# Kernel optimization log

Hardware: AMD Instinct MI355X
Metric: run time of the kernel (lower is better)

## Reference

```python
import jax, jax.numpy as jnp
import numpy as np

LN_EPS = 1e-5
NEG_INF = -1e38


def wkv_scan(w, u, k, v):
    """Numerically-stable RWKV WKV recurrence (matches wkv_cuda forward).
    w: [C] (negative decay), u: [C] bonus, k/v: [B,T,C]. Returns y: [B,T,C]."""
    Bdim, T, C = k.shape

    def step(carry, kv_t):
        p, q, o = carry  # running num, den, log-scale, each [B,C]
        kt, vt = kv_t
        no = jnp.maximum(o, u + kt)
        A = jnp.exp(o - no)
        Bw = jnp.exp(u + kt - no)
        y = (A * p + Bw * vt) / (A * q + Bw)
        no2 = jnp.maximum(w + o, kt)
        A2 = jnp.exp(w + o - no2)
        B2 = jnp.exp(kt - no2)
        return (A2 * p + B2 * vt, A2 * q + B2, no2), y

    init = (jnp.zeros((Bdim, C), k.dtype), jnp.zeros((Bdim, C), k.dtype),
            jnp.full((Bdim, C), NEG_INF, k.dtype))
    kT = jnp.moveaxis(k, 1, 0)  # [T,B,C]
    vT = jnp.moveaxis(v, 1, 0)
    _, ys = jax.lax.scan(step, init, (kT, vT))
    return jnp.moveaxis(ys, 0, 1)  # [B,T,C]


def setup_inputs() -> dict:
    key = jax.random.key(0)
    ks = jax.random.split(key, 8)
    B, C, H, W = 16, 192, 56, 56
    s = 0.02
    x = jax.random.normal(ks[0], (B, C, H, W), jnp.float32)
    Wk = jax.random.normal(ks[1], (C, C), jnp.float32) * s
    Wv = jax.random.normal(ks[2], (C, C), jnp.float32) * s
    Wr = jax.random.normal(ks[3], (C, C), jnp.float32) * s
    Wo = jax.random.normal(ks[4], (C, C), jnp.float32) * s
    ln_g = jnp.ones((C,), jnp.float32)
    ln_b = jnp.zeros((C,), jnp.float32)
    w_decay = -6.0 + 0.1 * jax.random.normal(ks[5], (C,), jnp.float32)
    u = 0.1 * jax.random.normal(ks[6], (C,), jnp.float32)
    return {"x": x, "Wk": Wk, "Wv": Wv, "Wr": Wr, "Wo": Wo,
            "ln_g": ln_g, "ln_b": ln_b, "w_decay": w_decay, "u": u}


def reference(x, Wk, Wv, Wr, Wo, ln_g, ln_b, w_decay, u):
    B, C, H, W = x.shape
    xs = jnp.transpose(x.reshape(B, C, H * W), (0, 2, 1))  # [B,T,C]
    k = jnp.einsum('btc,dc->btd', xs, Wk)
    v = jnp.einsum('btc,dc->btd', xs, Wv)
    r = jnp.einsum('btc,dc->btd', xs, Wr)
    real_w = -jnp.exp(w_decay)
    x_fwd = wkv_scan(real_w, u, k, v)
    x_bwd = jnp.flip(wkv_scan(real_w, u, jnp.flip(k, 1), jnp.flip(v, 1)), 1)
    x_bi = 0.5 * (x_fwd + x_bwd)
    h = jax.nn.sigmoid(r) * x_bi
    mu = jnp.mean(h, axis=-1, keepdims=True)
    var = jnp.var(h, axis=-1, keepdims=True)
    h = (h - mu) * jax.lax.rsqrt(var + LN_EPS) * ln_g + ln_b
    out = jnp.einsum('btc,dc->btd', h, Wo)  # dropout is identity at eval
    return jnp.transpose(out, (0, 2, 1)).reshape(B, C, H, W)
```

## Files before the change

kernel.cpp:

```cpp
#include <hip/hip_runtime.h>
#include <hip/hip_bf16.h>

#define BB 16
#define CC 192
#define TPIX 3136
#define NCH 49
#define CHL 64
#define NNELE ((size_t)BB * TPIX * CC)
#define NSTATE ((size_t)2 * BB * NCH * CC)
#define WCH (CC * CC)

typedef __attribute__((ext_vector_type(8))) short bf16x8;
typedef __attribute__((ext_vector_type(4))) float f32x4;
typedef __attribute__((ext_vector_type(16))) float f32x16;

__device__ __forceinline__ unsigned short f2bf(float f) {
    __hip_bfloat16 b = __float2bfloat16(f);
    return *reinterpret_cast<unsigned short*>(&b);
}
__device__ __forceinline__ float bf2f(unsigned short h) {
    union { unsigned u; float f; } v; v.u = ((unsigned)h) << 16;
    return v.f;
}


__global__ __launch_bounds__(256) void wcvt_frag(
    const float* __restrict__ Wk, const float* __restrict__ Wv,
    const float* __restrict__ Wr, const float* __restrict__ Wo,
    unsigned short* __restrict__ wfrag)
{
    const int id = blockIdx.x * 256 + threadIdx.x;
    const int m = id / 4608;
    const int r = id % 4608;
    const int tile = r >> 6;
    const int lane = r & 63;
    const int dr = tile / 12, tk = tile % 12;
    const int d = dr * 32 + (lane & 31);
    const int c = tk * 16 + (lane >> 5) * 8;
    const float* W = (m == 0) ? Wk : (m == 1) ? Wv : (m == 2) ? Wr : Wo;
    const float4 a = *(const float4*)&W[d * CC + c];
    const float4 b = *(const float4*)&W[d * CC + c + 4];
    bf16x8 o;
    o[0] = (short)f2bf(a.x); o[1] = (short)f2bf(a.y);
    o[2] = (short)f2bf(a.z); o[3] = (short)f2bf(a.w);
    o[4] = (short)f2bf(b.x); o[5] = (short)f2bf(b.y);
    o[6] = (short)f2bf(b.z); o[7] = (short)f2bf(b.w);
    *(bf16x8*)&wfrag[(size_t)m * WCH + (size_t)tile * 512 + lane * 8] = o;
}

__global__ __launch_bounds__(256) void xcvt_frag(
    const float* __restrict__ x, unsigned short* __restrict__ xfrag)
{
    const int t0 = blockIdx.x * 32;
    const int b  = blockIdx.y;
    __shared__ float ls[CC][33];
    const int tid = threadIdx.x;
#pragma unroll
    for (int it = 0; it < 6; ++it) {
        const int c  = it * 32 + (tid >> 3);
        const int t4 = (tid & 7) * 4;
        *(float4*)&ls[c][t4] =
            *(const float4*)&x[((size_t)b * CC + c) * TPIX + t0 + t4];
    }
    __syncthreads();
    const size_t tbase = ((size_t)(b * TPIX + t0) >> 5) * 12;
#pragma unroll
    for (int it = 0; it < 3; ++it) {
        const int id = it * 256 + tid;
        const int tk = id >> 6;
        const int lane = id & 63;
        const int r32 = lane & 31;
        const int c0 = tk * 16 + (lane >> 5) * 8;
        bf16x8 o;
#pragma unroll
        for (int e = 0; e < 8; ++e)
            o[e] = (short)f2bf(ls[c0 + e][r32]);
        *(bf16x8*)&xfrag[(tbase + tk) * 512 + lane * 8] = o;
    }
}

__global__ __launch_bounds__(512, 4) void proj_mfma32(
    const unsigned short* __restrict__ xfrag,
    const unsigned short* __restrict__ wfrag,
    unsigned short* __restrict__ kbf, unsigned short* __restrict__ vbf,
    unsigned short* __restrict__ rbf)
{
    __shared__ unsigned short wlds[WCH];
    const int tid  = threadIdx.x;
    const int lane = tid & 63;
    const int wv   = tid >> 6;
    const int tw   = wv >> 1;
    const int dwav = wv & 1;
    const int l31  = lane & 31;
    const int kh   = lane >> 5;
    const int m    = blockIdx.z;

    const size_t row0 = (size_t)blockIdx.x * 128 + tw * 32;
    const size_t xtb  = (row0 >> 5) * 12;

    bf16x8 xf[12];
#pragma unroll
    for (int ks = 0; ks < 12; ++ks)
        xf[ks] = *(const bf16x8*)&xfrag[(xtb + ks) * 512 + lane * 8];

    const unsigned short* wm = wfrag + (size_t)m * WCH;
#pragma unroll
    for (int it = 0; it < 9; ++it) {
        const int off = (it * 512 + tid) * 8;
        *(bf16x8*)&wlds[off] = *(const bf16x8*)&wm[off];
    }
    __syncthreads();

    f32x16 acc[3];
#pragma unroll
    for (int nn = 0; nn < 3; ++nn)
#pragma unroll
        for (int e = 0; e < 16; ++e) acc[nn][e] = 0.f;

#pragma unroll
    for (int ks = 0; ks < 12; ++ks) {
        bf16x8 wf[3];
#pragma unroll
        for (int nn = 0; nn < 3; ++nn)
            wf[nn] = *(const bf16x8*)&wlds[((dwav * 3 + nn) * 12 + ks) * 512 + lane * 8];
#pragma unroll
        for (int nn = 0; nn < 3; ++nn)
            acc[nn] = __builtin_amdgcn_mfma_f32_32x32x16_bf16(
                xf[ks], wf[nn], acc[nn], 0, 0, 0);
    }

    unsigned short* om = (m == 0) ? kbf : (m == 1) ? vbf : rbf;
#pragma unroll
    for (int nn = 0; nn < 3; ++nn) {
        const int d = dwav * 96 + nn * 32 + l31;
#pragma unroll
        for (int q = 0; q < 16; ++q) {
            const int t = (q & 3) + 8 * (q >> 2) + 4 * kh;
            om[(row0 + t) * CC + d] = f2bf(acc[nn][q]);
        }
    }
}

__global__ __launch_bounds__(512, 4) void outproj_mfma32(
    const unsigned short* __restrict__ hfrag,
    const unsigned short* __restrict__ wo,
    float* __restrict__ out)
{
    __shared__ unsigned short wlds[WCH];
    const int tid  = threadIdx.x;
    const int lane = tid & 63;
    const int wv   = tid >> 6;
    const int tw   = wv >> 1;
    const int dwav = wv & 1;
    const int l31  = lane & 31;
    const int kh   = lane >> 5;

    const size_t row0 = (size_t)blockIdx.x * 128 + tw * 32;
    const size_t htb  = (row0 >> 5) * 12;

    bf16x8 hf[12];
#pragma unroll
    for (int ks = 0; ks < 12; ++ks)
        hf[ks] = *(const bf16x8*)&hfrag[(htb + ks) * 512 + lane * 8];

#pragma unroll
    for (int it = 0; it < 9; ++it) {
        const int off = (it * 512 + tid) * 8;
        *(bf16x8*)&wlds[off] = *(const bf16x8*)&wo[off];
    }
    __syncthreads();

    f32x16 acc[3];
#pragma unroll
    for (int nn = 0; nn < 3; ++nn)
#pragma unroll
        for (int e = 0; e < 16; ++e) acc[nn][e] = 0.f;

#pragma unroll
    for (int ks = 0; ks < 12; ++ks) {
        bf16x8 wf[3];
#pragma unroll
        for (int nn = 0; nn < 3; ++nn)
            wf[nn] = *(const bf16x8*)&wlds[((dwav * 3 + nn) * 12 + ks) * 512 + lane * 8];
#pragma unroll
        for (int nn = 0; nn < 3; ++nn)
            acc[nn] = __builtin_amdgcn_mfma_f32_32x32x16_bf16(
                hf[ks], wf[nn], acc[nn], 0, 0, 0);
    }

#pragma unroll
    for (int nn = 0; nn < 3; ++nn) {
        const int d = dwav * 96 + nn * 32 + l31;
#pragma unroll
        for (int q2 = 0; q2 < 4; ++q2) {
            const size_t grow = row0 + 4 * kh + 8 * q2;
            const int b  = (int)(grow / TPIX);
            const int tl = (int)(grow % TPIX);
            f32x4 v4 = {acc[nn][q2 * 4 + 0], acc[nn][q2 * 4 + 1],
                        acc[nn][q2 * 4 + 2], acc[nn][q2 * 4 + 3]};
            *(f32x4*)&out[((size_t)b * CC + d) * TPIX + tl] = v4;
        }
    }
}

__global__ __launch_bounds__(256) void wkv_chunk_kernel(
    const unsigned short* __restrict__ kb, const unsigned short* __restrict__ vb,
    const float* __restrict__ wdec,
    float* __restrict__ sp, float* __restrict__ sq, float* __restrict__ so)
{
    const int gid = blockIdx.x * 256 + threadIdx.x;
    const int c  = gid % CC;
    const int r  = gid / CC;
    const int ch = r % NCH;
    const int r2 = r / NCH;
    const int b  = r2 % BB;
    const int dir = r2 / BB;

    const float w = -__expf(wdec[c]);
    const int tstart = dir ? (TPIX - 1 - ch * CHL) : (ch * CHL);
    const long stride = dir ? -(long)CC : (long)CC;
    long idx = ((long)b * TPIX + tstart) * CC + c;

    float p = 0.f, q = 0.f, o = -1e38f;
#pragma unroll 4
    for (int j = 0; j < CHL; ++j) {
        const float kt = bf2f(kb[idx]), vt = bf2f(vb[idx]);
        const float wo  = w + o;
        const float no2 = fmaxf(wo, kt);
        const float A2  = __expf(wo - no2);
        const float B2  = __expf(kt - no2);
        p = A2 * p + B2 * vt;
        q = A2 * q + B2;
        o = no2;
        idx += stride;
    }
    sp[gid] = p; sq[gid] = q; so[gid] = o;
}

__global__ __launch_bounds__(256) void wkv_prefix_kernel(
    float* __restrict__ sp, float* __restrict__ sq, float* __restrict__ so,
    const float* __restrict__ wdec)
{
    const int tid = blockIdx.x * 256 + threadIdx.x;
    if (tid >= 2 * BB * CC) return;
    const int c = tid % CC;
    const int g = tid / CC;
    const float w  = -__expf(wdec[c]);
    const float wL = w * CHL;

    float P = 0.f, Q = 0.f, O = -1e38f;
    size_t idx = (size_t)g * NCH * CC + c;
    for (int ch = 0; ch < NCH; ++ch) {
        const float pl = sp[idx], ql = sq[idx], ol = so[idx];
        sp[idx] = P; sq[idx] = Q; so[idx] = O;
        const float Ow = O + wL;
        const float no = fmaxf(Ow, ol);
        const float A  = __expf(Ow - no);
        const float Bf = __expf(ol - no);
        P = A * P + Bf * pl;
        Q = A * Q + Bf * ql;
        O = no;
        idx += CC;
    }
}

__global__ __launch_bounds__(256) void wkv_emit_kernel(
    const unsigned short* __restrict__ kb, const unsigned short* __restrict__ vb,
    const float* __restrict__ wdec, const float* __restrict__ ubias,
    const float* __restrict__ sp, const float* __restrict__ sq,
    const float* __restrict__ so,
    unsigned short* __restrict__ yfwd, unsigned short* __restrict__ ybwd)
{
    const int gid = blockIdx.x * 256 + threadIdx.x;
    const int c  = gid % CC;
    const int r  = gid / CC;
    const int ch = r % NCH;
    const int r2 = r / NCH;
    const int b  = r2 % BB;
    const int dir = r2 / BB;

    const float w = -__expf(wdec[c]);
    const float u = ubias[c];
    const int tstart = dir ? (TPIX - 1 - ch * CHL) : (ch * CHL);
    const long stride = dir ? -(long)CC : (long)CC;
    long idx = ((long)b * TPIX + tstart) * CC + c;
    unsigned short* yout = dir ? ybwd : yfwd;

    float p = sp[gid], q = sq[gid], o = so[gid];
#pragma unroll 2
    for (int j = 0; j < CHL; ++j) {
        const float kt = bf2f(kb[idx]), vt = bf2f(vb[idx]);
        const float uk  = u + kt;
        const float no  = fmaxf(o, uk);
        const float A   = __expf(o - no);
        const float Bw  = __expf(uk - no);
        const float num = A * p + Bw * vt;
        const float den = A * q + Bw;
        yout[idx] = f2bf(0.5f * __fdividef(num, den));
        const float wo  = w + o;
        const float no2 = fmaxf(wo, kt);
        const float A2  = __expf(wo - no2);
        const float B2  = __expf(kt - no2);
        p = A2 * p + B2 * vt;
        q = A2 * q + B2;
        o = no2;
        idx += stride;
    }
}

__global__ __launch_bounds__(192) void ln_kernel(
    const unsigned short* __restrict__ rbf,
    const unsigned short* __restrict__ yfwd, const unsigned short* __restrict__ ybwd,
    const float* __restrict__ gamma, const float* __restrict__ beta,
    unsigned short* __restrict__ hfrag)
{
    const size_t row = blockIdx.x;
    const int c = threadIdx.x;
    const size_t idx = row * CC + c;
    const float rv = bf2f(rbf[idx]);
    const float xb = bf2f(yfwd[idx]) + bf2f(ybwd[idx]);
    const float hv = xb / (1.f + __expf(-rv));
    float s = hv, s2 = hv * hv;
#pragma unroll
    for (int off = 1; off < 64; off <<= 1) {
        s  += __shfl_xor(s, off);
        s2 += __shfl_xor(s2, off);
    }
    __shared__ float red[2][3];
    const int wv = threadIdx.x >> 6;
    if ((threadIdx.x & 63) == 0) { red[0][wv] = s; red[1][wv] = s2; }
    __syncthreads();
    s  = red[0][0] + red[0][1] + red[0][2];
    s2 = red[1][0] + red[1][1] + red[1][2];
    const float mu   = s * (1.f / CC);
    const float var  = s2 * (1.f / CC) - mu * mu;
    const float rstd = rsqrtf(var + 1e-5f);
    const float hval = (hv - mu) * rstd * gamma[c] + beta[c];
    const size_t off = ((row >> 5) * 12 + (c >> 4)) * 512 +
                       ((row & 31) + ((c >> 3) & 1) * 32) * 8 + (c & 7);
    hfrag[off] = f2bf(hval);
}

extern "C" void kernel_launch(void* const* d_in, const int* in_sizes, int n_in,
                              void* d_out, int out_size, void* d_ws, size_t ws_size,
                              hipStream_t stream)
{
    const float* x    = (const float*)d_in[0];
    const float* Wk   = (const float*)d_in[1];
    const float* Wv   = (const float*)d_in[2];
    const float* Wr   = (const float*)d_in[3];
    const float* Wo   = (const float*)d_in[4];
    const float* ln_g = (const float*)d_in[5];
    const float* ln_b = (const float*)d_in[6];
    const float* wdec = (const float*)d_in[7];
    const float* u    = (const float*)d_in[8];

    unsigned short* kbf   = (unsigned short*)d_ws;
    unsigned short* vbf   = kbf + NNELE;
    unsigned short* rbf   = vbf + NNELE;
    unsigned short* xfrag = rbf + NNELE;
    unsigned short* wfrag = xfrag + NNELE;
    float* sp = (float*)xfrag;
    float* sq = sp + NSTATE;
    float* so = sq + NSTATE;
    unsigned short* hfrag = kbf;
    unsigned short* yfwd  = (unsigned short*)d_out;
    unsigned short* ybwd  = yfwd + NNELE;
    float* out = (float*)d_out;

    wcvt_frag<<<72, 256, 0, stream>>>(Wk, Wv, Wr, Wo, wfrag);
    xcvt_frag<<<dim3(TPIX / 32, BB), 256, 0, stream>>>(x, xfrag);

    proj_mfma32<<<dim3((BB * TPIX) / 128, 1, 3), 512, 0, stream>>>(
        xfrag, wfrag, kbf, vbf, rbf);

    const int nth = (int)NSTATE;
    wkv_chunk_kernel<<<nth / 256, 256, 0, stream>>>(kbf, vbf, wdec, sp, sq, so);
    wkv_prefix_kernel<<<(2 * BB * CC + 255) / 256, 256, 0, stream>>>(sp, sq, so, wdec);
    wkv_emit_kernel<<<nth / 256, 256, 0, stream>>>(kbf, vbf, wdec, u, sp, sq, so, yfwd, ybwd);

    ln_kernel<<<BB * TPIX, 192, 0, stream>>>(rbf, yfwd, ybwd, ln_g, ln_b, hfrag);

    outproj_mfma32<<<(BB * TPIX) / 128, 512, 0, stream>>>(hfrag, wfrag + 3 * WCH, out);
}
```

Baseline: 135.6 us.

## Fuse sigmoid-gate LayerNorm into output projection using MFMA fragment layout

The separate LayerNorm kernel is removed and its work moved into the output-projection MFMA kernel. To make this possible, the r projection and the WKV emit outputs are now written directly in the MFMA A-fragment layout. Each lane computes the gated value h for its 96 channels, and one shuffle across the two half-waves gives the row statistics. This drops a full-size launch and the hfrag round trip through memory. In exchange the emit kernel and the r projection now do scattered 2-byte stores, yfwd and ybwd move from the output buffer to the workspace, and h is rounded to bf16 before normalisation.

```diff
diff --git a/kernel.cpp b/kernel.cpp
--- a/kernel.cpp
+++ b/kernel.cpp
@@ -83,7 +83,7 @@
     const unsigned short* __restrict__ xfrag,
     const unsigned short* __restrict__ wfrag,
     unsigned short* __restrict__ kbf, unsigned short* __restrict__ vbf,
-    unsigned short* __restrict__ rbf)
+    unsigned short* __restrict__ rfrag)
 {
     __shared__ unsigned short wlds[WCH];
     const int tid  = threadIdx.x;
@@ -129,76 +129,28 @@
                 xf[ks], wf[nn], acc[nn], 0, 0, 0);
     }
 
-    unsigned short* om = (m == 0) ? kbf : (m == 1) ? vbf : rbf;
-#pragma unroll
-    for (int nn = 0; nn < 3; ++nn) {
-        const int d = dwav * 96 + nn * 32 + l31;
-#pragma unroll
-        for (int q = 0; q < 16; ++q) {
-            const int t = (q & 3) + 8 * (q >> 2) + 4 * kh;
-            om[(row0 + t) * CC + d] = f2bf(acc[nn][q]);
+    if (m == 2) {
+#pragma unroll
+        for (int nn = 0; nn < 3; ++nn) {
+            const int d = dwav * 96 + nn * 32 + l31;
+            const size_t tb = ((row0 >> 5) * 12 + (d >> 4)) * 512 +
+                              (size_t)(((d >> 3) & 1) * 32) * 8 + (d & 7);
+#pragma unroll
+            for (int q = 0; q < 16; ++q) {
+                const int tq = (q & 3) + 8 * (q >> 2) + 4 * kh;
+                rfrag[tb + tq * 8] = f2bf(acc[nn][q]);
+            }
         }
-    }
-}
-
-__global__ __launch_bounds__(512, 4) void outproj_mfma32(
-    const unsigned short* __restrict__ hfrag,
-    const unsigned short* __restrict__ wo,
-    float* __restrict__ out)
-{
-    __shared__ unsigned short wlds[WCH];
-    const int tid  = threadIdx.x;
-    const int lane = tid & 63;
-    const int wv   = tid >> 6;
-    const int tw   = wv >> 1;
-    const int dwav = wv & 1;
-    const int l31  = lane & 31;
-    const int kh   = lane >> 5;
-
-    const size_t row0 = (size_t)blockIdx.x * 128 + tw * 32;
-    const size_t htb  = (row0 >> 5) * 12;
-
-    bf16x8 hf[12];
-#pragma unroll
-    for (int ks = 0; ks < 12; ++ks)
-        hf[ks] = *(const bf16x8*)&hfrag[(htb + ks) * 512 + lane * 8];
-
-#pragma unroll
-    for (int it = 0; it < 9; ++it) {
-        const int off = (it * 512 + tid) * 8;
-        *(bf16x8*)&wlds[off] = *(const bf16x8*)&wo[off];
-    }
-    __syncthreads();
-
-    f32x16 acc[3];
-#pragma unroll
-    for (int nn = 0; nn < 3; ++nn)
-#pragma unroll
-        for (int e = 0; e < 16; ++e) acc[nn][e] = 0.f;
-
-#pragma unroll
-    for (int ks = 0; ks < 12; ++ks) {
-        bf16x8 wf[3];
-#pragma unroll
-        for (int nn = 0; nn < 3; ++nn)
-            wf[nn] = *(const bf16x8*)&wlds[((dwav * 3 + nn) * 12 + ks) * 512 + lane * 8];
-#pragma unroll
-        for (int nn = 0; nn < 3; ++nn)
-            acc[nn] = __builtin_amdgcn_mfma_f32_32x32x16_bf16(
-                hf[ks], wf[nn], acc[nn], 0, 0, 0);
-    }
-
-#pragma unroll
-    for (int nn = 0; nn < 3; ++nn) {
-        const int d = dwav * 96 + nn * 32 + l31;
-#pragma unroll
-        for (int q2 = 0; q2 < 4; ++q2) {
-            const size_t grow = row0 + 4 * kh + 8 * q2;
-            const int b  = (int)(grow / TPIX);
-            const int tl = (int)(grow % TPIX);
-            f32x4 v4 = {acc[nn][q2 * 4 + 0], acc[nn][q2 * 4 + 1],
-                        acc[nn][q2 * 4 + 2], acc[nn][q2 * 4 + 3]};
-            *(f32x4*)&out[((size_t)b * CC + d) * TPIX + tl] = v4;
+    } else {
+        unsigned short* om = (m == 0) ? kbf : vbf;
+#pragma unroll
+        for (int nn = 0; nn < 3; ++nn) {
+            const int d = dwav * 96 + nn * 32 + l31;
+#pragma unroll
+            for (int q = 0; q < 16; ++q) {
+                const int t = (q & 3) + 8 * (q >> 2) + 4 * kh;
+                om[(row0 + t) * CC + d] = f2bf(acc[nn][q]);
+            }
         }
     }
 }
@@ -283,8 +235,13 @@
     const float u = ubias[c];
     const int tstart = dir ? (TPIX - 1 - ch * CHL) : (ch * CHL);
     const long stride = dir ? -(long)CC : (long)CC;
+    const int rstep = dir ? -1 : 1;
     long idx = ((long)b * TPIX + tstart) * CC + c;
+    long row = (long)b * TPIX + tstart;
     unsigned short* yout = dir ? ybwd : yfwd;
+    const int ctile = c >> 4;
+    const int clane = ((c >> 3) & 1) * 32;
+    const int ce    = c & 7;
 
     float p = sp[gid], q = sq[gid], o = so[gid];
 #pragma unroll 2
@@ -296,7 +253,9 @@
         const float Bw  = __expf(uk - no);
         const float num = A * p + Bw * vt;
         const float den = A * q + Bw;
-        yout[idx] = f2bf(0.5f * __fdividef(num, den));
+        const size_t off = ((size_t)(row >> 5) * 12 + ctile) * 512 +
+                           (size_t)((row & 31) + clane) * 8 + ce;
+        yout[off] = f2bf(0.5f * __fdividef(num, den));
         const float wo  = w + o;
         const float no2 = fmaxf(wo, kt);
         const float A2  = __expf(wo - no2);
@@ -305,40 +264,113 @@
         q = A2 * q + B2;
         o = no2;
         idx += stride;
-    }
-}
-
-__global__ __launch_bounds__(192) void ln_kernel(
-    const unsigned short* __restrict__ rbf,
+        row += rstep;
+    }
+}
+
+__global__ __launch_bounds__(512) void outproj_ln_mfma32(
     const unsigned short* __restrict__ yfwd, const unsigned short* __restrict__ ybwd,
+    const unsigned short* __restrict__ rfrag,
     const float* __restrict__ gamma, const float* __restrict__ beta,
-    unsigned short* __restrict__ hfrag)
-{
-    const size_t row = blockIdx.x;
-    const int c = threadIdx.x;
-    const size_t idx = row * CC + c;
-    const float rv = bf2f(rbf[idx]);
-    const float xb = bf2f(yfwd[idx]) + bf2f(ybwd[idx]);
-    const float hv = xb / (1.f + __expf(-rv));
-    float s = hv, s2 = hv * hv;
-#pragma unroll
-    for (int off = 1; off < 64; off <<= 1) {
-        s  += __shfl_xor(s, off);
-        s2 += __shfl_xor(s2, off);
-    }
-    __shared__ float red[2][3];
-    const int wv = threadIdx.x >> 6;
-    if ((threadIdx.x & 63) == 0) { red[0][wv] = s; red[1][wv] = s2; }
+    const unsigned short* __restrict__ wo,
+    float* __restrict__ out)
+{
+    __shared__ unsigned short wlds[WCH];
+    __shared__ float gblds[CC];
+    __shared__ float bblds[CC];
+    const int tid  = threadIdx.x;
+    const int lane = tid & 63;
+    const int wv   = tid >> 6;
+    const int tw   = wv >> 1;
+    const int dwav = wv & 1;
+    const int l31  = lane & 31;
+    const int kh   = lane >> 5;
+
+#pragma unroll
+    for (int it = 0; it < 9; ++it) {
+        const int off = (it * 512 + tid) * 8;
+        *(bf16x8*)&wlds[off] = *(const bf16x8*)&wo[off];
+    }
+    if (tid < CC) { gblds[tid] = gamma[tid]; bblds[tid] = beta[tid]; }
     __syncthreads();
-    s  = red[0][0] + red[0][1] + red[0][2];
-    s2 = red[1][0] + red[1][1] + red[1][2];
+
+    const size_t row0 = (size_t)blockIdx.x * 128 + tw * 32;
+    const size_t htb  = (row0 >> 5) * 12;
+
+    bf16x8 hvb[12];
+    float s = 0.f, s2 = 0.f;
+#pragma unroll
+    for (int ks = 0; ks < 12; ++ks) {
+        const size_t fo = (htb + ks) * 512 + lane * 8;
+        const bf16x8 yf = *(const bf16x8*)&yfwd[fo];
+        const bf16x8 yb = *(const bf16x8*)&ybwd[fo];
+        const bf16x8 rv = *(const bf16x8*)&rfrag[fo];
+        bf16x8 hb;
+#pragma unroll
+        for (int e = 0; e < 8; ++e) {
+            const float xb = bf2f((unsigned short)yf[e]) + bf2f((unsigned short)yb[e]);
+            const float rr = bf2f((unsigned short)rv[e]);
+            const float h  = xb / (1.f + __expf(-rr));
+            s += h; s2 += h * h;
+            hb[e] = (short)f2bf(h);
+        }
+        hvb[ks] = hb;
+    }
+    s  += __shfl_xor(s, 32);
+    s2 += __shfl_xor(s2, 32);
     const float mu   = s * (1.f / CC);
     const float var  = s2 * (1.f / CC) - mu * mu;
     const float rstd = rsqrtf(var + 1e-5f);
-    const float hval = (hv - mu) * rstd * gamma[c] + beta[c];
-    const size_t off = ((row >> 5) * 12 + (c >> 4)) * 512 +
-                       ((row & 31) + ((c >> 3) & 1) * 32) * 8 + (c & 7);
-    hfrag[off] = f2bf(hval);
+
+#pragma unroll
+    for (int ks = 0; ks < 12; ++ks) {
+        const int cbase = ks * 16 + kh * 8;
+        const f32x4 g0 = *(const f32x4*)&gblds[cbase];
+        const f32x4 g1 = *(const f32x4*)&gblds[cbase + 4];
+        const f32x4 b0 = *(const f32x4*)&bblds[cbase];
+        const f32x4 b1 = *(const f32x4*)&bblds[cbase + 4];
+        bf16x8 hb = hvb[ks];
+#pragma unroll
+        for (int e = 0; e < 4; ++e) {
+            const float h0 = (bf2f((unsigned short)hb[e]) - mu) * rstd * g0[e] + b0[e];
+            const float h1 = (bf2f((unsigned short)hb[e + 4]) - mu) * rstd * g1[e] + b1[e];
+            hb[e]     = (short)f2bf(h0);
+            hb[e + 4] = (short)f2bf(h1);
+        }
+        hvb[ks] = hb;
+    }
+
+    f32x16 acc[3];
+#pragma unroll
+    for (int nn = 0; nn < 3; ++nn)
+#pragma unroll
+        for (int e = 0; e < 16; ++e) acc[nn][e] = 0.f;
+
+#pragma unroll
+    for (int ks = 0; ks < 12; ++ks) {
+        bf16x8 wf[3];
+#pragma unroll
+        for (int nn = 0; nn < 3; ++nn)
+            wf[nn] = *(const bf16x8*)&wlds[((dwav * 3 + nn) * 12 + ks) * 512 + lane * 8];
+#pragma unroll
+        for (int nn = 0; nn < 3; ++nn)
+            acc[nn] = __builtin_amdgcn_mfma_f32_32x32x16_bf16(
+                hvb[ks], wf[nn], acc[nn], 0, 0, 0);
+    }
+
+#pragma unroll
+    for (int nn = 0; nn < 3; ++nn) {
+        const int d = dwav * 96 + nn * 32 + l31;
+#pragma unroll
+        for (int q2 = 0; q2 < 4; ++q2) {
+            const size_t grow = row0 + 4 * kh + 8 * q2;
+            const int b  = (int)(grow / TPIX);
+            const int tl = (int)(grow % TPIX);
+            f32x4 v4 = {acc[nn][q2 * 4 + 0], acc[nn][q2 * 4 + 1],
+                        acc[nn][q2 * 4 + 2], acc[nn][q2 * 4 + 3]};
+            *(f32x4*)&out[((size_t)b * CC + d) * TPIX + tl] = v4;
+        }
+    }
 }
 
 extern "C" void kernel_launch(void* const* d_in, const int* in_sizes, int n_in,
@@ -357,29 +389,27 @@
 
     unsigned short* kbf   = (unsigned short*)d_ws;
     unsigned short* vbf   = kbf + NNELE;
-    unsigned short* rbf   = vbf + NNELE;
-    unsigned short* xfrag = rbf + NNELE;
+    unsigned short* rfrag = vbf + NNELE;
+    unsigned short* xfrag = rfrag + NNELE;
     unsigned short* wfrag = xfrag + NNELE;
+    unsigned short* yfwd  = wfrag + 4 * WCH;
+    unsigned short* ybwd  = yfwd + NNELE;
     float* sp = (float*)xfrag;
     float* sq = sp + NSTATE;
     float* so = sq + NSTATE;
-    unsigned short* hfrag = kbf;
-    unsigned short* yfwd  = (unsigned short*)d_out;
-    unsigned short* ybwd  = yfwd + NNELE;
     float* out = (float*)d_out;
 
     wcvt_frag<<<72, 256, 0, stream>>>(Wk, Wv, Wr, Wo, wfrag);
     xcvt_frag<<<dim3(TPIX / 32, BB), 256, 0, stream>>>(x, xfrag);
 
     proj_mfma32<<<dim3((BB * TPIX) / 128, 1, 3), 512, 0, stream>>>(
-        xfrag, wfrag, kbf, vbf, rbf);
+        xfrag, wfrag, kbf, vbf, rfrag);
 
     const int nth = (int)NSTATE;
     wkv_chunk_kernel<<<nth / 256, 256, 0, stream>>>(kbf, vbf, wdec, sp, sq, so);
     wkv_prefix_kernel<<<(2 * BB * CC + 255) / 256, 256, 0, stream>>>(sp, sq, so, wdec);
     wkv_emit_kernel<<<nth / 256, 256, 0, stream>>>(kbf, vbf, wdec, u, sp, sq, so, yfwd, ybwd);
 
-    ln_kernel<<<BB * TPIX, 192, 0, stream>>>(rbf, yfwd, ybwd, ln_g, ln_b, hfrag);
-
-    outproj_mfma32<<<(BB * TPIX) / 128, 512, 0, stream>>>(hfrag, wfrag + 3 * WCH, out);
-}
+    outproj_ln_mfma32<<<(BB * TPIX) / 128, 512, 0, stream>>>(
+        yfwd, ybwd, rfrag, ln_g, ln_b, wfrag + 3 * WCH, out);
+}
```

Measured after the change: 131.9 us. 1.03x faster.
